# Optimization experiments

Hardware: AMD Instinct MI355X
Metric: run time of the kernel (lower is better)

The kernel has to match this reference:

```python
import jax, jax.numpy as jnp
import numpy as np

N = 524288          # total nodes
B = 16384           # graphs in batch
E = 1048576         # directed edges (avg degree ~2)
NODE_F = 16
EDGE_F = 4
LATENT = 128
MAXN = 38
TRIU = MAXN * (MAXN + 1) // 2      # 741
MAXE = MAXN * (MAXN - 1) // 2      # 703


def _lin(k, fan_in, fan_out):
    kw, kb = jax.random.split(k)
    s = 1.0 / np.sqrt(fan_in)
    return (jax.random.uniform(kw, (fan_in, fan_out), jnp.float32, -s, s),
            jax.random.uniform(kb, (fan_out,), jnp.float32, -s, s))


def setup_inputs() -> dict:
    key = jax.random.key(0)
    ks = jax.random.split(key, 16)
    x = jax.random.normal(ks[0], (N, NODE_F), jnp.float32)
    edge_index = jax.random.randint(ks[1], (2, E), 0, N, jnp.int64)
    batch = jnp.repeat(jnp.arange(B, dtype=jnp.int64), N // B)
    eps = jax.random.normal(ks[2], (B, LATENT), jnp.float32)
    c1_w, c1_b = _lin(ks[3], NODE_F, 32)
    c2_w, c2_b = _lin(ks[4], 32, 64)
    fc1_w, fc1_b = _lin(ks[5], 64, 128)
    fc2_w, fc2_b = _lin(ks[6], 128, 2 * LATENT)
    d1_w, d1_b = _lin(ks[7], LATENT, 128)
    d2_w, d2_b = _lin(ks[8], 128, 256)
    d3_w, d3_b = _lin(ks[9], 256, 512)
    adj_w, adj_b = _lin(ks[10], 512, TRIU)
    node_w, node_b = _lin(ks[11], 512, MAXN * NODE_F)
    edgef_w, edgef_b = _lin(ks[12], 512, MAXE * EDGE_F)
    return dict(x=x, edge_index=edge_index, batch=batch, eps=eps,
                c1_w=c1_w, c1_b=c1_b, c2_w=c2_w, c2_b=c2_b,
                fc1_w=fc1_w, fc1_b=fc1_b, fc2_w=fc2_w, fc2_b=fc2_b,
                d1_w=d1_w, d1_b=d1_b, d1_g=jnp.ones(128), d1_bt=jnp.zeros(128),
                d2_w=d2_w, d2_b=d2_b, d2_g=jnp.ones(256), d2_bt=jnp.zeros(256),
                d3_w=d3_w, d3_b=d3_b, d3_g=jnp.ones(512), d3_bt=jnp.zeros(512),
                adj_w=adj_w, adj_b=adj_b, node_w=node_w, node_b=node_b,
                edgef_w=edgef_w, edgef_b=edgef_b)


def _gcn(x, W, b, src, dst):
    # PyG GCNConv default: x' = D^-1/2 (A + I) D^-1/2 (x W) + b
    h = x @ W
    loop = jnp.arange(N, dtype=src.dtype)
    s = jnp.concatenate([src, loop])
    d = jnp.concatenate([dst, loop])
    deg = jnp.zeros(N, h.dtype).at[d].add(1.0)
    dinv = jax.lax.rsqrt(deg)            # deg >= 1 due to self-loops
    norm = dinv[s] * dinv[d]
    out = jnp.zeros_like(h).at[d].add(norm[:, None] * h[s])
    return out + b


def _bn(h, g, bt):
    # BatchNorm1d in training mode: batch stats, biased variance, eps=1e-5
    m = h.mean(axis=0)
    v = jnp.mean((h - m) ** 2, axis=0)
    return g * (h - m) * jax.lax.rsqrt(v + 1e-5) + bt


def reference(x, edge_index, batch, eps,
              c1_w, c1_b, c2_w, c2_b, fc1_w, fc1_b, fc2_w, fc2_b,
              d1_w, d1_b, d1_g, d1_bt, d2_w, d2_b, d2_g, d2_bt,
              d3_w, d3_b, d3_g, d3_bt,
              adj_w, adj_b, node_w, node_b, edgef_w, edgef_b):
    src, dst = edge_index[0], edge_index[1]
    h = jax.nn.relu(_gcn(x, c1_w, c1_b, src, dst))
    h = _gcn(h, c2_w, c2_b, src, dst)
    # global mean pool over each graph
    ssum = jax.ops.segment_sum(h, batch, num_segments=B)
    cnt = jax.ops.segment_sum(jnp.ones((N, 1), h.dtype), batch, num_segments=B)
    g = ssum / jnp.maximum(cnt, 1.0)
    g = jax.nn.relu(g @ fc1_w + fc1_b)
    g = g @ fc2_w + fc2_b
    mu, log_sigma = g[:, :LATENT], g[:, LATENT:]
    z = eps * jnp.exp(log_sigma) + mu   # reparameterization
    h = jax.nn.relu(_bn(z @ d1_w + d1_b, d1_g, d1_bt))
    h = jax.nn.relu(_bn(h @ d2_w + d2_b, d2_g, d2_bt))
    h = jax.nn.relu(_bn(h @ d3_w + d3_b, d3_g, d3_bt))
    adj_triu = h @ adj_w + adj_b                                   # [B, 741]
    node_mat = (h @ node_w + node_b).reshape(-1, MAXN, NODE_F)     # [B, 38, 16]
    edge_triu = (h @ edgef_w + edgef_b).reshape(-1, MAXE, EDGE_F)  # [B, 703, 4]
    return adj_triu, node_mat, edge_triu
```

## Files before the change

kernel.cpp:

```cpp
#include <hip/hip_runtime.h>
#include <hip/hip_bf16.h>

#define N_NODES 524288
#define N_GRAPH 16384
#define N_EDGE  1048576
#define NPG     32
#define TRIU    741
#define NODE_COLS 608
#define EDGE_COLS 2812

typedef __attribute__((ext_vector_type(8))) short short8v;
typedef __attribute__((ext_vector_type(4))) float f32x4;
typedef unsigned short ushort_t;

__device__ __forceinline__ void gload16(const ushort_t* g, ushort_t* l) {
    __builtin_amdgcn_global_load_lds(
        (const __attribute__((address_space(1))) unsigned int*)g,
        (__attribute__((address_space(3))) unsigned int*)l, 16, 0, 0);
}

__device__ __forceinline__ float4 bf4_to_f4(uint2 u) {
    float4 r;
    r.x = __uint_as_float(u.x << 16);
    r.y = __uint_as_float(u.x & 0xffff0000u);
    r.z = __uint_as_float(u.y << 16);
    r.w = __uint_as_float(u.y & 0xffff0000u);
    return r;
}

__global__ __launch_bounds__(256) void k_degi(const int* __restrict__ ei, int* __restrict__ deg) {
    int e = blockIdx.x * 256 + threadIdx.x;
    if (e < N_EDGE) atomicAdd(&deg[ei[N_EDGE + e]], 1);
}

__global__ __launch_bounds__(256) void k_scan1(const int* __restrict__ deg, int* __restrict__ out,
                                               int* __restrict__ bsum) {
    __shared__ int wsum[4];
    int t = threadIdx.x;
    int base = blockIdx.x * 1024 + t * 4;
    int v0 = deg[base], v1 = deg[base + 1], v2 = deg[base + 2], v3 = deg[base + 3];
    int s = v0 + v1 + v2 + v3;
    int lane = t & 63, w = t >> 6;
    int incl = s;
#pragma unroll
    for (int off = 1; off < 64; off <<= 1) {
        int y = __shfl_up(incl, off, 64);
        if (lane >= off) incl += y;
    }
    if (lane == 63) wsum[w] = incl;
    __syncthreads();
    int wo = 0;
#pragma unroll
    for (int k = 0; k < 4; ++k) if (k < w) wo += wsum[k];
    int excl = wo + incl - s;
    out[base]     = excl;
    out[base + 1] = excl + v0;
    out[base + 2] = excl + v0 + v1;
    out[base + 3] = excl + v0 + v1 + v2;
    if (t == 255) bsum[blockIdx.x] = wo + incl;
}

__global__ __launch_bounds__(512) void k_scan2(int* __restrict__ bsum, float* __restrict__ stats) {
    __shared__ int wsum[8];
    int t = threadIdx.x, lane = t & 63, w = t >> 6;
    for (int j = t; j < 1792; j += 512) stats[j] = 0.f;
    int v = bsum[t];
    int incl = v;
#pragma unroll
    for (int off = 1; off < 64; off <<= 1) {
        int y = __shfl_up(incl, off, 64);
        if (lane >= off) incl += y;
    }
    if (lane == 63) wsum[w] = incl;
    __syncthreads();
    int wo = 0;
#pragma unroll
    for (int k = 0; k < 8; ++k) if (k < w) wo += wsum[k];
    bsum[t] = wo + incl - v;
}

__global__ __launch_bounds__(256) void k_scan3(int* __restrict__ out, const int* __restrict__ bsum,
                                               const int* __restrict__ deg, float* __restrict__ dinv,
                                               int* __restrict__ cnt) {
    int i = blockIdx.x * 256 + threadIdx.x;
    out[i] += bsum[i >> 10];
    dinv[i] = rsqrtf((float)deg[i] + 1.0f);
    cnt[i] = 0;
}

__global__ __launch_bounds__(256) void k_fill(const int* __restrict__ ei, const int* __restrict__ rowptr,
                                              int* __restrict__ cnt, int* __restrict__ perm) {
    int e = blockIdx.x * 256 + threadIdx.x;
    if (e >= N_EDGE) return;
    int s = ei[e], d = ei[N_EDGE + e];
    int p = rowptr[d] + atomicAdd(&cnt[d], 1);
    perm[p] = s;
}

__global__ __launch_bounds__(256) void k_gx1(const float* __restrict__ x, const float* __restrict__ dinv,
                                             const int* __restrict__ rowptr, const int* __restrict__ deg,
                                             const int* __restrict__ perm, const float* __restrict__ W,
                                             const float* __restrict__ b1, ushort_t* __restrict__ hs) {
    __shared__ float Ws[16 * 32];
    __shared__ float bs[32];
    __shared__ float Acc[64][17];
    int t = threadIdx.x;
    for (int j = t; j < 512; j += 256) Ws[j] = W[j];
    if (t < 32) bs[t] = b1[t];
    int q = t & 3;
    int r = t >> 2;
    size_t i = (size_t)blockIdx.x * 64 + r;
    int st = rowptr[i], c = deg[i];
    float di = dinv[i];
    float4 s = *(const float4*)(x + i * 16 + q * 4);
    s.x *= di; s.y *= di; s.z *= di; s.w *= di;
    for (int e = 0; e < c; ++e) {
        int src = perm[st + e];
        float ds = dinv[src];
        float4 v = *(const float4*)(x + (size_t)src * 16 + q * 4);
        s.x += ds * v.x; s.y += ds * v.y; s.z += ds * v.z; s.w += ds * v.w;
    }
    Acc[r][q * 4]     = s.x;
    Acc[r][q * 4 + 1] = s.y;
    Acc[r][q * 4 + 2] = s.z;
    Acc[r][q * 4 + 3] = s.w;
    __syncthreads();
    float o[8];
#pragma unroll
    for (int j = 0; j < 8; ++j) o[j] = bs[q * 8 + j];
#pragma unroll
    for (int k = 0; k < 16; ++k) {
        float xv = Acc[r][k] * di;
#pragma unroll
        for (int j = 0; j < 8; ++j) o[j] += xv * Ws[k * 32 + q * 8 + j];
    }
    ushort_t os[8];
#pragma unroll
    for (int j = 0; j < 8; ++j) {
        float v = fmaxf(o[j], 0.f) * di;
        __hip_bfloat16 b = __float2bfloat16(v);
        os[j] = *(ushort_t*)&b;
    }
    *(uint4*)(hs + i * 32 + q * 8) = *(uint4*)os;
}

__global__ __launch_bounds__(256) void k_gpool(const ushort_t* __restrict__ hs, const float* __restrict__ dinv,
                                               const int* __restrict__ rowptr, const int* __restrict__ perm,
                                               float* __restrict__ pooled) {
    __shared__ int rp[33];
    __shared__ float4 partv[32][8];
    int G = blockIdx.x;
    int t = threadIdx.x;
    int grp = t >> 3;
    int q = t & 7;
    if (t < 33) rp[t] = rowptr[G * 32 + t];
    __syncthreads();
    int node = G * 32 + grp;
    float dd = dinv[node];
    int st = rp[grp], en = rp[grp + 1];
    float4 v = bf4_to_f4(*(const uint2*)(hs + (size_t)node * 32 + q * 4));
    for (int p = st; p < en; ++p) {
        int s = perm[p];
        float4 u = bf4_to_f4(*(const uint2*)(hs + (size_t)s * 32 + q * 4));
        v.x += u.x; v.y += u.y; v.z += u.z; v.w += u.w;
    }
    v.x *= dd; v.y *= dd; v.z *= dd; v.w *= dd;
    partv[grp][q] = v;
    __syncthreads();
#pragma unroll
    for (int s = 16; s > 0; s >>= 1) {
        if (grp < s) {
            float4 o = partv[grp + s][q];
            float4 m = partv[grp][q];
            m.x += o.x; m.y += o.y; m.z += o.z; m.w += o.w;
            partv[grp][q] = m;
        }
        __syncthreads();
    }
    if (t < 32) pooled[(size_t)G * 32 + t] = ((const float*)&partv[0][0])[t] * (1.f / NPG);
}

__global__ __launch_bounds__(256) void k_enc(const float* __restrict__ pooled, const float* __restrict__ c2w,
                                             const float* __restrict__ c2b, const float* __restrict__ fc1w,
                                             const float* __restrict__ fc1b, const float* __restrict__ fc2w,
                                             const float* __restrict__ fc2b, const float* __restrict__ eps,
                                             ushort_t* __restrict__ zb) {
    __shared__ float W1s[32 * 64];
    __shared__ float W2s[64 * 128];
    __shared__ float b1s[64], b2s[128];
    __shared__ float Gs[64][65];
    __shared__ float Hs[64][129];
    __shared__ float Bs[16][256];
    int t = threadIdx.x;
    for (int j = t; j < 2048; j += 256) W1s[j] = c2w[j];
    for (int j = t; j < 8192; j += 256) W2s[j] = fc1w[j];
    if (t < 64) b1s[t] = c2b[t];
    if (t < 128) b2s[t] = fc1b[t];
    __syncthreads();
    size_t r0 = (size_t)blockIdx.x * 64;
    for (int e = t; e < 64 * 64; e += 256) {
        int r = e >> 6, c = e & 63;
        const float* pr = pooled + (r0 + r) * 32;
        float s = b1s[c];
#pragma unroll
        for (int k = 0; k < 32; ++k) s += pr[k] * W1s[k * 64 + c];
        Gs[r][c] = s;
    }
    __syncthreads();
    for (int e = t; e < 64 * 128; e += 256) {
        int r = e >> 7, j = e & 127;
        float s = b2s[j];
#pragma unroll
        for (int k = 0; k < 64; ++k) s += Gs[r][k] * W2s[k * 128 + j];
        Hs[r][j] = fmaxf(s, 0.f);
    }
    int tr = t >> 5;
    int tc = t & 31;
    float acc[8][8];
#pragma unroll
    for (int i = 0; i < 8; ++i)
#pragma unroll
        for (int j = 0; j < 8; ++j) acc[i][j] = 0.f;
    for (int k0 = 0; k0 < 128; k0 += 16) {
        __syncthreads();
#pragma unroll
        for (int l = 0; l < 16; ++l) {
            int idx = t + l * 256;
            int kk = idx >> 8, c = idx & 255;
            Bs[kk][c] = fc2w[(size_t)(k0 + kk) * 256 + c];
        }
        __syncthreads();
#pragma unroll
        for (int kk = 0; kk < 16; ++kk) {
            float a[8], b[8];
#pragma unroll
            for (int i = 0; i < 8; ++i) a[i] = Hs[tr * 8 + i][k0 + kk];
#pragma unroll
            for (int j = 0; j < 4; ++j) { b[j] = Bs[kk][tc * 4 + j]; b[j + 4] = Bs[kk][128 + tc * 4 + j]; }
#pragma unroll
            for (int i = 0; i < 8; ++i)
#pragma unroll
                for (int j = 0; j < 8; ++j) acc[i][j] += a[i] * b[j];
        }
    }
#pragma unroll
    for (int i = 0; i < 8; ++i) {
        size_t row = r0 + tr * 8 + i;
        ushort_t os[4];
#pragma unroll
        for (int j = 0; j < 4; ++j) {
            int c = tc * 4 + j;
            float mu = acc[i][j] + fc2b[c];
            float ls = acc[i][j + 4] + fc2b[128 + c];
            float z = eps[row * 128 + c] * expf(ls) + mu;
            __hip_bfloat16 b = __float2bfloat16(z);
            os[j] = *(ushort_t*)&b;
        }
        *(uint2*)(zb + row * 128 + tc * 4) = *(uint2*)os;
    }
}

template<int MODE>
__device__ __forceinline__ void mgemm_core(const ushort_t* __restrict__ A, const ushort_t* __restrict__ Wt,
                                           const float* __restrict__ bias, float* __restrict__ Cf,
                                           ushort_t* __restrict__ Cb, float* __restrict__ ssum,
                                           float* __restrict__ ssq, int K, int Nc,
                                           size_t row0, int col0, ushort_t* As, ushort_t* Bs) {
    const int tid = threadIdx.x;
    const int lane = tid & 63;
    const int wave = tid >> 6;
    const int wm = (wave >> 1) * 64, wn = (wave & 1) * 64;

    const int rl = lane >> 3;
    const int sl = lane & 7;
    const int ss = sl ^ rl;
    const ushort_t* ga = A  + (row0 + wave * 32 + rl) * (size_t)K + ss * 8;
    const ushort_t* gb = Wt + (size_t)(wave * 32 + rl) * K + ss * 8;

    const int l15 = lane & 15;
    const int lkg = lane >> 4;
    const int lr4 = lkg * 4;

    f32x4 acc[4][4];
#pragma unroll
    for (int m = 0; m < 4; ++m)
#pragma unroll
        for (int n = 0; n < 4; ++n) acc[m][n] = (f32x4)0.f;

    for (int k0 = 0; k0 < K; k0 += 64) {
        __syncthreads();
#pragma unroll
        for (int j = 0; j < 4; ++j) {
            gload16(ga + k0 + (size_t)(j * 8) * K, &As[(wave * 32 + j * 8) * 64]);
            gload16(gb + k0 + (size_t)(j * 8) * K, &Bs[(wave * 32 + j * 8) * 64]);
        }
        asm volatile("s_waitcnt vmcnt(0)" ::: "memory");
        __syncthreads();
#pragma unroll
        for (int kk = 0; kk < 2; ++kk) {
            short8v af[4], bf[4];
#pragma unroll
            for (int m = 0; m < 4; ++m) {
                int r = wm + m * 16 + l15;
                int s = (kk * 4 + lkg) ^ (r & 7);
                af[m] = *(const short8v*)&As[r * 64 + s * 8];
            }
#pragma unroll
            for (int n = 0; n < 4; ++n) {
                int r = wn + n * 16 + l15;
                int s = (kk * 4 + lkg) ^ (r & 7);
                bf[n] = *(const short8v*)&Bs[r * 64 + s * 8];
            }
#pragma unroll
            for (int m = 0; m < 4; ++m)
#pragma unroll
                for (int n = 0; n < 4; ++n)
                    acc[m][n] = __builtin_amdgcn_mfma_f32_16x16x32_bf16(af[m], bf[n], acc[m][n], 0, 0, 0);
        }
    }

#pragma unroll
    for (int n = 0; n < 4; ++n) {
        int col = col0 + wn + n * 16 + l15;
        if (MODE == 0) {
            bool ok = col < Nc;
            float bv = ok ? bias[col] : 0.f;
#pragma unroll
            for (int m = 0; m < 4; ++m) {
                size_t rbase = (row0 + wm + m * 16 + lr4) * (size_t)Nc + col;
                if (ok) {
#pragma unroll
                    for (int j = 0; j < 4; ++j)
                        Cf[rbase + (size_t)j * Nc] = acc[m][n][j] + bv;
                }
            }
        } else {
            float bv = bias[col];
            float cs = 0.f, cq = 0.f;
#pragma unroll
            for (int m = 0; m < 4; ++m) {
                size_t rbase = (row0 + wm + m * 16 + lr4) * (size_t)Nc + col;
#pragma unroll
                for (int j = 0; j < 4; ++j) {
                    float v = acc[m][n][j] + bv;
                    __hip_bfloat16 b = __float2bfloat16(v);
                    Cb[rbase + (size_t)j * Nc] = *(ushort_t*)&b;
                    cs += v; cq += v * v;
                }
            }
            cs += __shfl_xor(cs, 16, 64);  cq += __shfl_xor(cq, 16, 64);
            cs += __shfl_xor(cs, 32, 64);  cq += __shfl_xor(cq, 32, 64);
            if (lane < 16) {
                atomicAdd(&ssum[col], cs);
                atomicAdd(&ssq[col], cq);
            }
        }
    }
}

__global__ __launch_bounds__(256, 3) void k_mgemm1(const ushort_t* __restrict__ A, const ushort_t* __restrict__ Wt,
                                                   const float* __restrict__ bias, ushort_t* __restrict__ Cb,
                                                   float* __restrict__ ssum, float* __restrict__ ssq,
                                                   int K, int Nc) {
    __shared__ ushort_t As[128 * 64];
    __shared__ ushort_t Bs[128 * 64];
    int col0 = blockIdx.x * 128;
    mgemm_core<1>(A, Wt + (size_t)col0 * K, bias, nullptr, Cb, ssum, ssq,
                  K, Nc, (size_t)blockIdx.y * 128, col0, As, Bs);
}

__global__ __launch_bounds__(256, 3) void k_heads(const ushort_t* __restrict__ A, const ushort_t* __restrict__ WtBase,
                                                  const float* __restrict__ adj_b, const float* __restrict__ node_b,
                                                  const float* __restrict__ edge_b, float* __restrict__ out) {
    __shared__ ushort_t As[128 * 64];
    __shared__ ushort_t Bs[128 * 64];
    int id = blockIdx.x;
    int swz = (id & 7) * 528 + (id >> 3);
    int by = swz / 33, hx = swz % 33;
    const float* bias; float* outp; int Nc, col0;
    if (hx < 6)       { bias = adj_b;  outp = out;                                  Nc = TRIU;      col0 = hx * 128; }
    else if (hx < 11) { bias = node_b; outp = out + (size_t)N_GRAPH * TRIU;         Nc = NODE_COLS; col0 = (hx - 6) * 128; }
    else              { bias = edge_b; outp = out + (size_t)N_GRAPH * (TRIU + NODE_COLS); Nc = EDGE_COLS; col0 = (hx - 11) * 128; }
    mgemm_core<0>(A, WtBase + (size_t)(hx * 128) * 512, bias, outp, nullptr, nullptr, nullptr,
                  512, Nc, (size_t)by * 128, col0, As, Bs);
}

__global__ __launch_bounds__(256) void k_wt_all(const float* __restrict__ d1w, const float* __restrict__ d2w,
                                                const float* __restrict__ d3w, const float* __restrict__ adjw,
                                                const float* __restrict__ nodw, const float* __restrict__ edgw,
                                                ushort_t* __restrict__ wt1, ushort_t* __restrict__ wt2,
                                                ushort_t* __restrict__ wt3, ushort_t* __restrict__ wta,
                                                ushort_t* __restrict__ wtn, ushort_t* __restrict__ wte) {
    __shared__ ushort_t t[32][33];
    int id = blockIdx.x;
    const float* W; ushort_t* Wt; int K, Nc, gx, lid;
    if (id < 16)        { W = d1w;  Wt = wt1; K = 128; Nc = 128;       gx = 4;  lid = id; }
    else if (id < 48)   { W = d2w;  Wt = wt2; K = 128; Nc = 256;       gx = 8;  lid = id - 16; }
    else if (id < 176)  { W = d3w;  Wt = wt3; K = 256; Nc = 512;       gx = 16; lid = id - 48; }
    else if (id < 560)  { W = adjw; Wt = wta; K = 512; Nc = TRIU;      gx = 24; lid = id - 176; }
    else if (id < 880)  { W = nodw; Wt = wtn; K = 512; Nc = NODE_COLS; gx = 20; lid = id - 560; }
    else                { W = edgw; Wt = wte; K = 512; Nc = EDGE_COLS; gx = 88; lid = id - 880; }
    int c0 = (lid % gx) * 32, k0 = (lid / gx) * 32;
    int tx = threadIdx.x & 31, ty = threadIdx.x >> 5;
#pragma unroll
    for (int i = 0; i < 4; ++i) {
        int k = k0 + ty + i * 8;
        int c = c0 + tx;
        float v = (c < Nc) ? W[(size_t)k * Nc + c] : 0.f;
        __hip_bfloat16 b = __float2bfloat16(v);
        t[ty + i * 8][tx] = *(ushort_t*)&b;
    }
    __syncthreads();
#pragma unroll
    for (int i = 0; i < 4; ++i) {
        int c = c0 + ty + i * 8;
        Wt[(size_t)c * K + k0 + tx] = t[tx][ty + i * 8];
    }
}

__global__ __launch_bounds__(256) void k_bnb(const ushort_t* __restrict__ Y, const float* __restrict__ ssum,
                                             const float* __restrict__ ssq, const float* __restrict__ gm,
                                             const float* __restrict__ bt, ushort_t* __restrict__ A,
                                             int cmask) {
    int idx8 = blockIdx.x * 256 + threadIdx.x;
    int base = idx8 * 8;
    int c0 = base & cmask;
    uint4 in = *(const uint4*)(Y + base);
    ushort_t ys[8];
    *(uint4*)ys = in;
    ushort_t os[8];
#pragma unroll
    for (int k = 0; k < 8; ++k) {
        int c = c0 + k;
        float m = ssum[c] * (1.f / N_GRAPH);
        float v = ssq[c] * (1.f / N_GRAPH) - m * m;
        float h = __bfloat162float(*(__hip_bfloat16*)&ys[k]);
        float hn = (h - m) * rsqrtf(v + 1e-5f) * gm[c] + bt[c];
        __hip_bfloat16 b = __float2bfloat16(fmaxf(hn, 0.f));
        os[k] = *(ushort_t*)&b;
    }
    *(uint4*)(A + base) = *(uint4*)os;
}

extern "C" void kernel_launch(void* const* d_in, const int* in_sizes, int n_in,
                              void* d_out, int out_size, void* d_ws, size_t ws_size,
                              hipStream_t stream) {
    const float* x      = (const float*)d_in[0];
    const int*   ei     = (const int*)d_in[1];
    const float* eps    = (const float*)d_in[3];
    const float* c1_w   = (const float*)d_in[4];
    const float* c1_b   = (const float*)d_in[5];
    const float* c2_w   = (const float*)d_in[6];
    const float* c2_b   = (const float*)d_in[7];
    const float* fc1_w  = (const float*)d_in[8];
    const float* fc1_b  = (const float*)d_in[9];
    const float* fc2_w  = (const float*)d_in[10];
    const float* fc2_b  = (const float*)d_in[11];
    const float* d1_w   = (const float*)d_in[12];
    const float* d1_b   = (const float*)d_in[13];
    const float* d1_g   = (const float*)d_in[14];
    const float* d1_bt  = (const float*)d_in[15];
    const float* d2_w   = (const float*)d_in[16];
    const float* d2_b   = (const float*)d_in[17];
    const float* d2_g   = (const float*)d_in[18];
    const float* d2_bt  = (const float*)d_in[19];
    const float* d3_w   = (const float*)d_in[20];
    const float* d3_b   = (const float*)d_in[21];
    const float* d3_g   = (const float*)d_in[22];
    const float* d3_bt  = (const float*)d_in[23];
    const float* adj_w  = (const float*)d_in[24];
    const float* adj_b  = (const float*)d_in[25];
    const float* node_w = (const float*)d_in[26];
    const float* node_b = (const float*)d_in[27];
    const float* edgef_w = (const float*)d_in[28];
    const float* edgef_b = (const float*)d_in[29];
    float* out = (float*)d_out;

    const size_t Nn = N_NODES, Bg = N_GRAPH;
    float* R    = (float*)d_ws;
    ushort_t* hs = (ushort_t*)R;
    float* dinv = R + Nn * 128;
    float* stats = dinv + Nn;
    float* s1 = stats,       *q1 = stats + 128;
    float* s2 = stats + 256, *q2 = stats + 512;
    float* s3 = stats + 768, *q3 = stats + 1280;
    int* degi   = (int*)(stats + 2048);
    int* rowptr = degi + Nn;
    int* cnt    = rowptr + Nn;
    int* perm   = cnt + Nn;
    int* bsum   = perm + N_EDGE;
    float* pooled = (float*)(bsum + 512);
    ushort_t* zb  = (ushort_t*)(R + Bg * 128);
    ushort_t* y1  = (ushort_t*)(R + Bg * 192);
    ushort_t* a1b = (ushort_t*)(R + Bg * 256);
    ushort_t* y2  = (ushort_t*)(R + Bg * 320);
    ushort_t* a2b = (ushort_t*)(R + Bg * 448);
    ushort_t* y3  = (ushort_t*)(R + Bg * 576);
    ushort_t* a3b = (ushort_t*)(R + Bg * 832);
    ushort_t* wt_d1  = (ushort_t*)(R + Bg * 1792);
    ushort_t* wt_d2  = wt_d1 + 128 * 128;
    ushort_t* wt_d3  = wt_d2 + 256 * 128;
    ushort_t* wt_adj = wt_d3 + 512 * 256;
    ushort_t* wt_nod = wt_adj + 768 * 512;
    ushort_t* wt_edg = wt_nod + 640 * 512;

    hipMemsetAsync(degi, 0, Nn * sizeof(int), stream);
    k_degi<<<N_EDGE / 256, 256, 0, stream>>>(ei, degi);
    k_scan1<<<N_NODES / 1024, 256, 0, stream>>>(degi, rowptr, bsum);
    k_scan2<<<1, 512, 0, stream>>>(bsum, stats);
    k_scan3<<<N_NODES / 256, 256, 0, stream>>>(rowptr, bsum, degi, dinv, cnt);
    k_fill<<<N_EDGE / 256, 256, 0, stream>>>(ei, rowptr, cnt, perm);

    k_gx1<<<N_NODES / 64, 256, 0, stream>>>(x, dinv, rowptr, degi, perm, c1_w, c1_b, hs);
    k_gpool<<<N_GRAPH, 256, 0, stream>>>(hs, dinv, rowptr, perm, pooled);

    k_enc<<<N_GRAPH / 64, 256, 0, stream>>>(pooled, c2_w, c2_b, fc1_w, fc1_b, fc2_w, fc2_b, eps, zb);

    k_wt_all<<<2288, 256, 0, stream>>>(d1_w, d2_w, d3_w, adj_w, node_w, edgef_w,
                                       wt_d1, wt_d2, wt_d3, wt_adj, wt_nod, wt_edg);

    k_mgemm1<<<dim3(1, N_GRAPH / 128), 256, 0, stream>>>(zb, wt_d1, d1_b, y1, s1, q1, 128, 128);
    k_bnb<<<N_GRAPH * 128 / 8 / 256, 256, 0, stream>>>(y1, s1, q1, d1_g, d1_bt, a1b, 127);
    k_mgemm1<<<dim3(2, N_GRAPH / 128), 256, 0, stream>>>(a1b, wt_d2, d2_b, y2, s2, q2, 128, 256);
    k_bnb<<<N_GRAPH * 256 / 8 / 256, 256, 0, stream>>>(y2, s2, q2, d2_g, d2_bt, a2b, 255);
    k_mgemm1<<<dim3(4, N_GRAPH / 128), 256, 0, stream>>>(a2b, wt_d3, d3_b, y3, s3, q3, 256, 512);
    k_bnb<<<N_GRAPH * 512 / 8 / 256, 256, 0, stream>>>(y3, s3, q3, d3_g, d3_bt, a3b, 511);

    k_heads<<<4224, 256, 0, stream>>>(a3b, wt_adj, adj_b, node_b, edgef_b, out);

    (void)in_sizes; (void)n_in; (void)out_size; (void)ws_size;
}
```

Measured before the change: 479.8 us.

## Fuse batchnorm into GEMM A-loads, merge scan stages and weight transpose

Drops the separate batchnorm+ReLU kernels by having each following GEMM compute per-column scale and shift and apply them while staging A tiles into LDS through registers. Folds the second scan pass into scan1 using a last-block atomic counter, and merges the weight transpose into the pooling launch as extra blocks. Stages the head GEMM output through LDS so global stores are coalesced float4 writes. This removes several launches and the intermediate activation round trips, but A staging loses the async global_load_lds path and adds per-element ALU work.

```diff
diff --git a/kernel.cpp b/kernel.cpp
--- a/kernel.cpp
+++ b/kernel.cpp
@@ -34,8 +34,10 @@
 }
 
 __global__ __launch_bounds__(256) void k_scan1(const int* __restrict__ deg, int* __restrict__ out,
-                                               int* __restrict__ bsum) {
+                                               int* __restrict__ bsum, int* __restrict__ ctr,
+                                               float* __restrict__ stats) {
     __shared__ int wsum[4];
+    __shared__ int lastf;
     int t = threadIdx.x;
     int base = blockIdx.x * 1024 + t * 4;
     int v0 = deg[base], v1 = deg[base + 1], v2 = deg[base + 2], v3 = deg[base + 3];
@@ -57,26 +59,33 @@
     out[base + 1] = excl + v0;
     out[base + 2] = excl + v0 + v1;
     out[base + 3] = excl + v0 + v1 + v2;
-    if (t == 255) bsum[blockIdx.x] = wo + incl;
-}
-
-__global__ __launch_bounds__(512) void k_scan2(int* __restrict__ bsum, float* __restrict__ stats) {
-    __shared__ int wsum[8];
-    int t = threadIdx.x, lane = t & 63, w = t >> 6;
-    for (int j = t; j < 1792; j += 512) stats[j] = 0.f;
-    int v = bsum[t];
-    int incl = v;
+    if (t == 255) {
+        bsum[blockIdx.x] = wo + incl;
+        __threadfence();
+        lastf = (atomicAdd(ctr, 1) == gridDim.x - 1);
+    }
+    __syncthreads();
+    if (!lastf) return;
+    __threadfence();
+    for (int j = t; j < 1792; j += 256) stats[j] = 0.f;
+    int b0 = atomicAdd(&bsum[2 * t], 0);
+    int b1 = atomicAdd(&bsum[2 * t + 1], 0);
+    int s2 = b0 + b1;
+    int incl2 = s2;
 #pragma unroll
     for (int off = 1; off < 64; off <<= 1) {
-        int y = __shfl_up(incl, off, 64);
-        if (lane >= off) incl += y;
-    }
-    if (lane == 63) wsum[w] = incl;
-    __syncthreads();
-    int wo = 0;
-#pragma unroll
-    for (int k = 0; k < 8; ++k) if (k < w) wo += wsum[k];
-    bsum[t] = wo + incl - v;
+        int y = __shfl_up(incl2, off, 64);
+        if (lane >= off) incl2 += y;
+    }
+    __shared__ int wsum2[4];
+    if (lane == 63) wsum2[w] = incl2;
+    __syncthreads();
+    int wo2 = 0;
+#pragma unroll
+    for (int k = 0; k < 4; ++k) if (k < w) wo2 += wsum2[k];
+    int excl2 = wo2 + incl2 - s2;
+    bsum[2 * t]     = excl2;
+    bsum[2 * t + 1] = excl2 + b0;
 }
 
 __global__ __launch_bounds__(256) void k_scan3(int* __restrict__ out, const int* __restrict__ bsum,
@@ -144,13 +153,47 @@
     *(uint4*)(hs + i * 32 + q * 8) = *(uint4*)os;
 }
 
-__global__ __launch_bounds__(256) void k_gpool(const ushort_t* __restrict__ hs, const float* __restrict__ dinv,
-                                               const int* __restrict__ rowptr, const int* __restrict__ perm,
-                                               float* __restrict__ pooled) {
+__global__ __launch_bounds__(256) void k_gpool_wt(const ushort_t* __restrict__ hs, const float* __restrict__ dinv,
+                                                  const int* __restrict__ rowptr, const int* __restrict__ perm,
+                                                  float* __restrict__ pooled,
+                                                  const float* __restrict__ d1w, const float* __restrict__ d2w,
+                                                  const float* __restrict__ d3w, const float* __restrict__ adjw,
+                                                  const float* __restrict__ nodw, const float* __restrict__ edgw,
+                                                  ushort_t* __restrict__ wt1, ushort_t* __restrict__ wt2,
+                                                  ushort_t* __restrict__ wt3, ushort_t* __restrict__ wta,
+                                                  ushort_t* __restrict__ wtn, ushort_t* __restrict__ wte) {
     __shared__ int rp[33];
     __shared__ float4 partv[32][8];
+    __shared__ ushort_t tt[32][33];
+    int t = threadIdx.x;
+    if (blockIdx.x >= N_GRAPH) {
+        int id = blockIdx.x - N_GRAPH;
+        const float* W; ushort_t* Wt; int K, Nc, gx, lid;
+        if (id < 16)        { W = d1w;  Wt = wt1; K = 128; Nc = 128;       gx = 4;  lid = id; }
+        else if (id < 48)   { W = d2w;  Wt = wt2; K = 128; Nc = 256;       gx = 8;  lid = id - 16; }
+        else if (id < 176)  { W = d3w;  Wt = wt3; K = 256; Nc = 512;       gx = 16; lid = id - 48; }
+        else if (id < 560)  { W = adjw; Wt = wta; K = 512; Nc = TRIU;      gx = 24; lid = id - 176; }
+        else if (id < 880)  { W = nodw; Wt = wtn; K = 512; Nc = NODE_COLS; gx = 20; lid = id - 560; }
+        else                { W = edgw; Wt = wte; K = 512; Nc = EDGE_COLS; gx = 88; lid = id - 880; }
+        int c0 = (lid % gx) * 32, k0 = (lid / gx) * 32;
+        int tx = t & 31, ty = t >> 5;
+#pragma unroll
+        for (int i = 0; i < 4; ++i) {
+            int k = k0 + ty + i * 8;
+            int c = c0 + tx;
+            float v = (c < Nc) ? W[(size_t)k * Nc + c] : 0.f;
+            __hip_bfloat16 b = __float2bfloat16(v);
+            tt[ty + i * 8][tx] = *(ushort_t*)&b;
+        }
+        __syncthreads();
+#pragma unroll
+        for (int i = 0; i < 4; ++i) {
+            int c = c0 + ty + i * 8;
+            Wt[(size_t)c * K + k0 + tx] = tt[tx][ty + i * 8];
+        }
+        return;
+    }
     int G = blockIdx.x;
-    int t = threadIdx.x;
     int grp = t >> 3;
     int q = t & 7;
     if (t < 33) rp[t] = rowptr[G * 32 + t];
@@ -190,7 +233,7 @@
     __shared__ float b1s[64], b2s[128];
     __shared__ float Gs[64][65];
     __shared__ float Hs[64][129];
-    __shared__ float Bs[16][256];
+    __shared__ float Bss[16][256];
     int t = threadIdx.x;
     for (int j = t; j < 2048; j += 256) W1s[j] = c2w[j];
     for (int j = t; j < 8192; j += 256) W2s[j] = fc1w[j];
@@ -227,7 +270,7 @@
         for (int l = 0; l < 16; ++l) {
             int idx = t + l * 256;
             int kk = idx >> 8, c = idx & 255;
-            Bs[kk][c] = fc2w[(size_t)(k0 + kk) * 256 + c];
+            Bss[kk][c] = fc2w[(size_t)(k0 + kk) * 256 + c];
         }
         __syncthreads();
 #pragma unroll
@@ -236,7 +279,7 @@
 #pragma unroll
             for (int i = 0; i < 8; ++i) a[i] = Hs[tr * 8 + i][k0 + kk];
 #pragma unroll
-            for (int j = 0; j < 4; ++j) { b[j] = Bs[kk][tc * 4 + j]; b[j + 4] = Bs[kk][128 + tc * 4 + j]; }
+            for (int j = 0; j < 4; ++j) { b[j] = Bss[kk][tc * 4 + j]; b[j + 4] = Bss[kk][128 + tc * 4 + j]; }
 #pragma unroll
             for (int i = 0; i < 8; ++i)
 #pragma unroll
@@ -260,12 +303,15 @@
     }
 }
 
-template<int MODE>
+template<int MODE, int NORM>
 __device__ __forceinline__ void mgemm_core(const ushort_t* __restrict__ A, const ushort_t* __restrict__ Wt,
                                            const float* __restrict__ bias, float* __restrict__ Cf,
                                            ushort_t* __restrict__ Cb, float* __restrict__ ssum,
-                                           float* __restrict__ ssq, int K, int Nc,
-                                           size_t row0, int col0, ushort_t* As, ushort_t* Bs) {
+                                           float* __restrict__ ssq,
+                                           const float* __restrict__ nsum, const float* __restrict__ nsq,
+                                           const float* __restrict__ ng, const float* __restrict__ nbt,
+                                           int K, int Nc, size_t row0, int col0,
+                                           ushort_t* As, ushort_t* Bs, float* scs, float* shs) {
     const int tid = threadIdx.x;
     const int lane = tid & 63;
     const int wave = tid >> 6;
@@ -274,13 +320,27 @@
     const int rl = lane >> 3;
     const int sl = lane & 7;
     const int ss = sl ^ rl;
-    const ushort_t* ga = A  + (row0 + wave * 32 + rl) * (size_t)K + ss * 8;
     const ushort_t* gb = Wt + (size_t)(wave * 32 + rl) * K + ss * 8;
 
     const int l15 = lane & 15;
     const int lkg = lane >> 4;
     const int lr4 = lkg * 4;
 
+    const int ar = tid >> 1;
+    const int ah = (tid & 1) * 32;
+    const ushort_t* ga = NORM ? (A + (row0 + ar) * (size_t)K + ah)
+                              : (A + (row0 + wave * 32 + rl) * (size_t)K + ss * 8);
+
+    if (NORM) {
+        for (int c = tid; c < K; c += 256) {
+            float m = nsum[c] * (1.f / N_GRAPH);
+            float v = nsq[c] * (1.f / N_GRAPH) - m * m;
+            float sc = ng[c] * rsqrtf(v + 1e-5f);
+            scs[c] = sc;
+            shs[c] = nbt[c] - m * sc;
+        }
+    }
+
     f32x4 acc[4][4];
 #pragma unroll
     for (int m = 0; m < 4; ++m)
@@ -288,12 +348,39 @@
         for (int n = 0; n < 4; ++n) acc[m][n] = (f32x4)0.f;
 
     for (int k0 = 0; k0 < K; k0 += 64) {
+        uint4 av[4];
+        if (NORM) {
+            av[0] = *(const uint4*)(ga + k0);
+            av[1] = *(const uint4*)(ga + k0 + 8);
+            av[2] = *(const uint4*)(ga + k0 + 16);
+            av[3] = *(const uint4*)(ga + k0 + 24);
+        }
         __syncthreads();
-#pragma unroll
-        for (int j = 0; j < 4; ++j) {
-            gload16(ga + k0 + (size_t)(j * 8) * K, &As[(wave * 32 + j * 8) * 64]);
+        if (NORM) {
+#pragma unroll
+            for (int j = 0; j < 4; ++j) {
+                ushort_t in8[8];
+                *(uint4*)in8 = av[j];
+                ushort_t ob[8];
+#pragma unroll
+                for (int e = 0; e < 8; ++e) {
+                    int kidx = k0 + ah + j * 8 + e;
+                    float h = __uint_as_float(((unsigned)in8[e]) << 16);
+                    float hn = fmaxf(h * scs[kidx] + shs[kidx], 0.f);
+                    __hip_bfloat16 b = __float2bfloat16(hn);
+                    ob[e] = *(ushort_t*)&b;
+                }
+                int slot = ((ah >> 3) + j) ^ (ar & 7);
+                *(uint4*)&As[ar * 64 + slot * 8] = *(uint4*)ob;
+            }
+        } else {
+#pragma unroll
+            for (int j = 0; j < 4; ++j)
+                gload16(ga + k0 + (size_t)(j * 8) * K, &As[(wave * 32 + j * 8) * 64]);
+        }
+#pragma unroll
+        for (int j = 0; j < 4; ++j)
             gload16(gb + k0 + (size_t)(j * 8) * K, &Bs[(wave * 32 + j * 8) * 64]);
-        }
         asm volatile("s_waitcnt vmcnt(0)" ::: "memory");
         __syncthreads();
 #pragma unroll
@@ -319,30 +406,58 @@
         }
     }
 
-#pragma unroll
-    for (int n = 0; n < 4; ++n) {
-        int col = col0 + wn + n * 16 + l15;
-        if (MODE == 0) {
-            bool ok = col < Nc;
-            float bv = ok ? bias[col] : 0.f;
+    if (MODE == 0) {
+        float* Cs = (float*)As;
+        float bv[4];
+#pragma unroll
+        for (int n = 0; n < 4; ++n) {
+            int col = col0 + wn + n * 16 + l15;
+            bv[n] = (col < Nc) ? bias[col] : 0.f;
+        }
+#pragma unroll
+        for (int h = 0; h < 2; ++h) {
+            __syncthreads();
+            if ((wave >> 1) == h) {
+#pragma unroll
+                for (int m = 0; m < 4; ++m)
+#pragma unroll
+                    for (int n = 0; n < 4; ++n)
+#pragma unroll
+                        for (int j = 0; j < 4; ++j)
+                            Cs[(m * 16 + lr4 + j) * 128 + wn + n * 16 + l15] = acc[m][n][j] + bv[n];
+            }
+            __syncthreads();
+            if ((Nc & 3) == 0) {
+#pragma unroll
+                for (int i = 0; i < 8; ++i) {
+                    int f = tid + i * 256;
+                    int r = f >> 5, c4 = (f & 31) << 2;
+                    int col = col0 + c4;
+                    size_t row = row0 + h * 64 + r;
+                    if (col < Nc) *(float4*)&Cf[row * Nc + col] = *(float4*)&Cs[r * 128 + c4];
+                }
+            } else {
+#pragma unroll 4
+                for (int i = 0; i < 32; ++i) {
+                    int f = tid + i * 256;
+                    int r = f >> 7, c = f & 127;
+                    int col = col0 + c;
+                    if (col < Nc) Cf[(row0 + h * 64 + (size_t)r) * Nc + col] = Cs[r * 128 + c];
+                }
+            }
+        }
+    } else {
+#pragma unroll
+        for (int n = 0; n < 4; ++n) {
+            int col = col0 + wn + n * 16 + l15;
+            float bvv = bias[col];
+            float cs = 0.f, cq = 0.f;
 #pragma unroll
             for (int m = 0; m < 4; ++m) {
                 size_t rbase = (row0 + wm + m * 16 + lr4) * (size_t)Nc + col;
-                if (ok) {
-#pragma unroll
-                    for (int j = 0; j < 4; ++j)
-                        Cf[rbase + (size_t)j * Nc] = acc[m][n][j] + bv;
-                }
-            }
-        } else {
-            float bv = bias[col];
-            float cs = 0.f, cq = 0.f;
-#pragma unroll
-            for (int m = 0; m < 4; ++m) {
-                size_t rbase = (row0 + wm + m * 16 + lr4) * (size_t)Nc + col;
 #pragma unroll
                 for (int j = 0; j < 4; ++j) {
-                    float v = acc[m][n][j] + bv;
+                    float v = acc[m][n][j] + bvv;
                     __hip_bfloat16 b = __float2bfloat16(v);
                     Cb[rbase + (size_t)j * Nc] = *(ushort_t*)&b;
                     cs += v; cq += v * v;
@@ -358,88 +473,43 @@
     }
 }
 
+template<int NORM>
 __global__ __launch_bounds__(256, 3) void k_mgemm1(const ushort_t* __restrict__ A, const ushort_t* __restrict__ Wt,
                                                    const float* __restrict__ bias, ushort_t* __restrict__ Cb,
                                                    float* __restrict__ ssum, float* __restrict__ ssq,
+                                                   const float* __restrict__ nsum, const float* __restrict__ nsq,
+                                                   const float* __restrict__ ng, const float* __restrict__ nbt,
                                                    int K, int Nc) {
-    __shared__ ushort_t As[128 * 64];
-    __shared__ ushort_t Bs[128 * 64];
+    __shared__ unsigned long long smem[4608];
+    ushort_t* As = (ushort_t*)smem;
+    ushort_t* Bs = As + 128 * 64;
+    float* scs = (float*)(Bs + 128 * 64);
+    float* shs = scs + 512;
     int col0 = blockIdx.x * 128;
-    mgemm_core<1>(A, Wt + (size_t)col0 * K, bias, nullptr, Cb, ssum, ssq,
-                  K, Nc, (size_t)blockIdx.y * 128, col0, As, Bs);
+    mgemm_core<1, NORM>(A, Wt + (size_t)col0 * K, bias, nullptr, Cb, ssum, ssq,
+                        nsum, nsq, ng, nbt, K, Nc, (size_t)blockIdx.y * 128, col0, As, Bs, scs, shs);
 }
 
 __global__ __launch_bounds__(256, 3) void k_heads(const ushort_t* __restrict__ A, const ushort_t* __restrict__ WtBase,
                                                   const float* __restrict__ adj_b, const float* __restrict__ node_b,
-                                                  const float* __restrict__ edge_b, float* __restrict__ out) {
-    __shared__ ushort_t As[128 * 64];
-    __shared__ ushort_t Bs[128 * 64];
+                                                  const float* __restrict__ edge_b,
+                                                  const float* __restrict__ nsum, const float* __restrict__ nsq,
+                                                  const float* __restrict__ ng, const float* __restrict__ nbt,
+                                                  float* __restrict__ out) {
+    __shared__ unsigned long long smem[4608];
+    ushort_t* As = (ushort_t*)smem;
+    ushort_t* Bs = As + 128 * 64;
+    float* scs = (float*)(Bs + 128 * 64);
+    float* shs = scs + 512;
     int id = blockIdx.x;
     int swz = (id & 7) * 528 + (id >> 3);
     int by = swz / 33, hx = swz % 33;
     const float* bias; float* outp; int Nc, col0;
-    if (hx < 6)       { bias = adj_b;  outp = out;                                  Nc = TRIU;      col0 = hx * 128; }
-    else if (hx < 11) { bias = node_b; outp = out + (size_t)N_GRAPH * TRIU;         Nc = NODE_COLS; col0 = (hx - 6) * 128; }
+    if (hx < 6)       { bias = adj_b;  outp = out;                                        Nc = TRIU;      col0 = hx * 128; }
+    else if (hx < 11) { bias = node_b; outp = out + (size_t)N_GRAPH * TRIU;               Nc = NODE_COLS; col0 = (hx - 6) * 128; }
     else              { bias = edge_b; outp = out + (size_t)N_GRAPH * (TRIU + NODE_COLS); Nc = EDGE_COLS; col0 = (hx - 11) * 128; }
-    mgemm_core<0>(A, WtBase + (size_t)(hx * 128) * 512, bias, outp, nullptr, nullptr, nullptr,
-                  512, Nc, (size_t)by * 128, col0, As, Bs);
-}
-
-__global__ __launch_bounds__(256) void k_wt_all(const float* __restrict__ d1w, const float* __restrict__ d2w,
-                                                const float* __restrict__ d3w, const float* __restrict__ adjw,
-                                                const float* __restrict__ nodw, const float* __restrict__ edgw,
-                                                ushort_t* __restrict__ wt1, ushort_t* __restrict__ wt2,
-                                                ushort_t* __restrict__ wt3, ushort_t* __restrict__ wta,
-                                                ushort_t* __restrict__ wtn, ushort_t* __restrict__ wte) {
-    __shared__ ushort_t t[32][33];
-    int id = blockIdx.x;
-    const float* W; ushort_t* Wt; int K, Nc, gx, lid;
-    if (id < 16)        { W = d1w;  Wt = wt1; K = 128; Nc = 128;       gx = 4;  lid = id; }
-    else if (id < 48)   { W = d2w;  Wt = wt2; K = 128; Nc = 256;       gx = 8;  lid = id - 16; }
-    else if (id < 176)  { W = d3w;  Wt = wt3; K = 256; Nc = 512;       gx = 16; lid = id - 48; }
-    else if (id < 560)  { W = adjw; Wt = wta; K = 512; Nc = TRIU;      gx = 24; lid = id - 176; }
-    else if (id < 880)  { W = nodw; Wt = wtn; K = 512; Nc = NODE_COLS; gx = 20; lid = id - 560; }
-    else                { W = edgw; Wt = wte; K = 512; Nc = EDGE_COLS; gx = 88; lid = id - 880; }
-    int c0 = (lid % gx) * 32, k0 = (lid / gx) * 32;
-    int tx = threadIdx.x & 31, ty = threadIdx.x >> 5;
-#pragma unroll
-    for (int i = 0; i < 4; ++i) {
-        int k = k0 + ty + i * 8;
-        int c = c0 + tx;
-        float v = (c < Nc) ? W[(size_t)k * Nc + c] : 0.f;
-        __hip_bfloat16 b = __float2bfloat16(v);
-        t[ty + i * 8][tx] = *(ushort_t*)&b;
-    }
-    __syncthreads();
-#pragma unroll
-    for (int i = 0; i < 4; ++i) {
-        int c = c0 + ty + i * 8;
-        Wt[(size_t)c * K + k0 + tx] = t[tx][ty + i * 8];
-    }
-}
-
-__global__ __launch_bounds__(256) void k_bnb(const ushort_t* __restrict__ Y, const float* __restrict__ ssum,
-                                             const float* __restrict__ ssq, const float* __restrict__ gm,
-                                             const float* __restrict__ bt, ushort_t* __restrict__ A,
-                                             int cmask) {
-    int idx8 = blockIdx.x * 256 + threadIdx.x;
-    int base = idx8 * 8;
-    int c0 = base & cmask;
-    uint4 in = *(const uint4*)(Y + base);
-    ushort_t ys[8];
-    *(uint4*)ys = in;
-    ushort_t os[8];
-#pragma unroll
-    for (int k = 0; k < 8; ++k) {
-        int c = c0 + k;
-        float m = ssum[c] * (1.f / N_GRAPH);
-        float v = ssq[c] * (1.f / N_GRAPH) - m * m;
-        float h = __bfloat162float(*(__hip_bfloat16*)&ys[k]);
-        float hn = (h - m) * rsqrtf(v + 1e-5f) * gm[c] + bt[c];
-        __hip_bfloat16 b = __float2bfloat16(fmaxf(hn, 0.f));
-        os[k] = *(ushort_t*)&b;
-    }
-    *(uint4*)(A + base) = *(uint4*)os;
+    mgemm_core<0, 1>(A, WtBase + (size_t)(hx * 128) * 512, bias, outp, nullptr, nullptr, nullptr,
+                     nsum, nsq, ng, nbt, 512, Nc, (size_t)by * 128, col0, As, Bs, scs, shs);
 }
 
 extern "C" void kernel_launch(void* const* d_in, const int* in_sizes, int n_in,
@@ -485,18 +555,16 @@
     float* s2 = stats + 256, *q2 = stats + 512;
     float* s3 = stats + 768, *q3 = stats + 1280;
     int* degi   = (int*)(stats + 2048);
-    int* rowptr = degi + Nn;
+    int* ctr    = degi + Nn;
+    int* rowptr = ctr + 16;
     int* cnt    = rowptr + Nn;
     int* perm   = cnt + Nn;
     int* bsum   = perm + N_EDGE;
     float* pooled = (float*)(bsum + 512);
     ushort_t* zb  = (ushort_t*)(R + Bg * 128);
     ushort_t* y1  = (ushort_t*)(R + Bg * 192);
-    ushort_t* a1b = (ushort_t*)(R + Bg * 256);
     ushort_t* y2  = (ushort_t*)(R + Bg * 320);
-    ushort_t* a2b = (ushort_t*)(R + Bg * 448);
     ushort_t* y3  = (ushort_t*)(R + Bg * 576);
-    ushort_t* a3b = (ushort_t*)(R + Bg * 832);
     ushort_t* wt_d1  = (ushort_t*)(R + Bg * 1792);
     ushort_t* wt_d2  = wt_d1 + 128 * 128;
     ushort_t* wt_d3  = wt_d2 + 256 * 128;
@@ -504,29 +572,27 @@
     ushort_t* wt_nod = wt_adj + 768 * 512;
     ushort_t* wt_edg = wt_nod + 640 * 512;
 
-    hipMemsetAsync(degi, 0, Nn * sizeof(int), stream);
+    hipMemsetAsync(degi, 0, (Nn + 16) * sizeof(int), stream);
     k_degi<<<N_EDGE / 256, 256, 0, stream>>>(ei, degi);
-    k_scan1<<<N_NODES / 1024, 256, 0, stream>>>(degi, rowptr, bsum);
-    k_scan2<<<1, 512, 0, stream>>>(bsum, stats);
+    k_scan1<<<N_NODES / 1024, 256, 0, stream>>>(degi, rowptr, bsum, ctr, stats);
     k_scan3<<<N_NODES / 256, 256, 0, stream>>>(rowptr, bsum, degi, dinv, cnt);
     k_fill<<<N_EDGE / 256, 256, 0, stream>>>(ei, rowptr, cnt, perm);
 
     k_gx1<<<N_NODES / 64, 256, 0, stream>>>(x, dinv, rowptr, degi, perm, c1_w, c1_b, hs);
-    k_gpool<<<N_GRAPH, 256, 0, stream>>>(hs, dinv, rowptr, perm, pooled);
+    k_gpool_wt<<<N_GRAPH + 2288, 256, 0, stream>>>(hs, dinv, rowptr, perm, pooled,
+                                                   d1_w, d2_w, d3_w, adj_w, node_w, edgef_w,
+                                                   wt_d1, wt_d2, wt_d3, wt_adj, wt_nod, wt_edg);
 
     k_enc<<<N_GRAPH / 64, 256, 0, stream>>>(pooled, c2_w, c2_b, fc1_w, fc1_b, fc2_w, fc2_b, eps, zb);
 
-    k_wt_all<<<2288, 256, 0, stream>>>(d1_w, d2_w, d3_w, adj_w, node_w, edgef_w,
-                                       wt_d1, wt_d2, wt_d3, wt_adj, wt_nod, wt_edg);
-
-    k_mgemm1<<<dim3(1, N_GRAPH / 128), 256, 0, stream>>>(zb, wt_d1, d1_b, y1, s1, q1, 128, 128);
-    k_bnb<<<N_GRAPH * 128 / 8 / 256, 256, 0, stream>>>(y1, s1, q1, d1_g, d1_bt, a1b, 127);
-    k_mgemm1<<<dim3(2, N_GRAPH / 128), 256, 0, stream>>>(a1b, wt_d2, d2_b, y2, s2, q2, 128, 256);
-    k_bnb<<<N_GRAPH * 256 / 8 / 256, 256, 0, stream>>>(y2, s2, q2, d2_g, d2_bt, a2b, 255);
-    k_mgemm1<<<dim3(4, N_GRAPH / 128), 256, 0, stream>>>(a2b, wt_d3, d3_b, y3, s3, q3, 256, 512);
-    k_bnb<<<N_GRAPH * 512 / 8 / 256, 256, 0, stream>>>(y3, s3, q3, d3_g, d3_bt, a3b, 511);
-
-    k_heads<<<4224, 256, 0, stream>>>(a3b, wt_adj, adj_b, node_b, edgef_b, out);
+    k_mgemm1<0><<<dim3(1, N_GRAPH / 128), 256, 0, stream>>>(zb, wt_d1, d1_b, y1, s1, q1,
+                                                            nullptr, nullptr, nullptr, nullptr, 128, 128);
+    k_mgemm1<1><<<dim3(2, N_GRAPH / 128), 256, 0, stream>>>(y1, wt_d2, d2_b, y2, s2, q2,
+                                                            s1, q1, d1_g, d1_bt, 128, 256);
+    k_mgemm1<1><<<dim3(4, N_GRAPH / 128), 256, 0, stream>>>(y2, wt_d3, d3_b, y3, s3, q3,
+                                                            s2, q2, d2_g, d2_bt, 256, 512);
+
+    k_heads<<<4224, 256, 0, stream>>>(y3, wt_adj, adj_b, node_b, edgef_b, s3, q3, d3_g, d3_bt, out);
 
     (void)in_sizes; (void)n_in; (void)out_size; (void)ws_size;
 }
```

After: 443.3 us. 7.6% less time.
